# Kernel optimization log

Measured on AMD Instinct MI355X. Metric: run time of the kernel, lower is better.

The kernel has to match this reference:

```python
import jax, jax.numpy as jnp
import numpy as np

B, N, E = 2, 2048, 2048
HQ, HKV, D = 32, 8, 64
SCALE = 1.0 / np.sqrt(D)


def setup_inputs() -> dict:
    key = jax.random.key(0)
    ks = jax.random.split(key, 9)
    s = lambda k, shape, fan: jax.random.normal(k, shape, jnp.float32) / np.sqrt(fan)
    return {
        "x": jax.random.normal(ks[0], (B, N, E), jnp.float32),
        "Wq": s(ks[1], (HQ * D, E), E),
        "bq": jnp.zeros((HQ * D,), jnp.float32),
        "Wk": s(ks[2], (HKV * D, E), E),
        "bk": jnp.zeros((HKV * D,), jnp.float32),
        "Wv": s(ks[3], (HKV * D, E), E),
        "bv": jnp.zeros((HKV * D,), jnp.float32),
        "Wo": s(ks[4], (E, E), E),
        "bo": jnp.zeros((E,), jnp.float32),
    }


def _attention(x, Wq, bq, Wk, bk, Wv, bv, Wo, bo):
    G = HQ // HKV  # query heads per kv head
    # projections (torch Linear: y = x @ W.T + b)
    q = (jnp.einsum("bne,fe->bnf", x, Wq) + bq).reshape(B, N, HKV, G, D)
    k = (jnp.einsum("bne,fe->bnf", x, Wk) + bk).reshape(B, N, HKV, D)
    v = (jnp.einsum("bne,fe->bnf", x, Wv) + bv).reshape(B, N, HKV, D)
    # scores [B, HKV, G, N, N] -- GQA without materializing repeated K/V
    scores = jnp.einsum("bnhgd,bmhd->bhgnm", q, k) * SCALE
    causal = jnp.tril(jnp.ones((N, N), bool))
    scores = jnp.where(causal, scores, -jnp.inf)
    p = jax.nn.softmax(scores, axis=-1)
    o = jnp.einsum("bhgnm,bmhd->bnhgd", p, v).reshape(B, N, E)
    return jnp.einsum("bne,fe->bnf", o, Wo) + bo


def reference(x, Wq, bq, Wk, bk, Wv, bv, Wo, bo):
    return _attention(x, Wq, bq, Wk, bk, Wv, bv, Wo, bo)
```

## Files before the change

kernel.cpp:

```cpp
#include <hip/hip_runtime.h>
#include <hip/hip_bf16.h>


#define B_   2
#define N_   2048
#define E_   2048
#define HQ_  32
#define HKV_ 8
#define D_   64
#define BN_  (B_*N_)

typedef __attribute__((ext_vector_type(8))) short bf16x8;
typedef __attribute__((ext_vector_type(4))) float f32x4;

#define MFMA16(a,b,c) __builtin_amdgcn_mfma_f32_16x16x32_bf16(a,b,c,0,0,0)

__device__ inline unsigned short f2bf(float f) {
  unsigned u = __builtin_bit_cast(unsigned, f);
  u += 0x7FFFu + ((u >> 16) & 1u);
  return (unsigned short)(u >> 16);
}

__device__ inline unsigned pack_bf16_trunc(float lo, float hi) {
  return __builtin_amdgcn_perm(__builtin_bit_cast(unsigned, hi),
                               __builtin_bit_cast(unsigned, lo), 0x07060302u);
}

__device__ inline void gload_lds16(const void* g, void* l) {
  __builtin_amdgcn_global_load_lds(
      (const __attribute__((address_space(1))) void*)g,
      (__attribute__((address_space(3))) void*)l, 16, 0, 0);
}

__global__ void cast_all(const float* __restrict__ x,  const float* __restrict__ wq,
                         const float* __restrict__ wk, const float* __restrict__ wv,
                         const float* __restrict__ wo, unsigned short* __restrict__ dst) {
  const int c0 = 2097152;
  const int c1 = c0 + 1048576;
  const int c2 = c1 + 262144;
  const int c3 = c2 + 262144;
  const int c4 = c3 + 1048576;
  int i = blockIdx.x * blockDim.x + threadIdx.x;
  const int stride = gridDim.x * blockDim.x;
  for (; i < c4; i += stride) {
    const float* src; int off;
    if      (i < c0) { src = x;  off = i; }
    else if (i < c1) { src = wq; off = i - c0; }
    else if (i < c2) { src = wk; off = i - c1; }
    else if (i < c3) { src = wv; off = i - c2; }
    else             { src = wo; off = i - c3; }
    float4 f = reinterpret_cast<const float4*>(src)[off];
    ushort4 u;
    u.x = f2bf(f.x); u.y = f2bf(f.y); u.z = f2bf(f.z); u.w = f2bf(f.w);
    reinterpret_cast<ushort4*>(dst)[i] = u;
  }
}

__global__ __launch_bounds__(512, 4) void gemm_qkv(
    const unsigned short* __restrict__ A,
    const unsigned short* __restrict__ Wq, const unsigned short* __restrict__ Wk,
    const unsigned short* __restrict__ Wv,
    const float* __restrict__ bq, const float* __restrict__ bk, const float* __restrict__ bv,
    unsigned short* __restrict__ Qo, unsigned short* __restrict__ Ko,
    unsigned short* __restrict__ Vto)
{
  __shared__ __align__(16) unsigned short As[2][8192];
  __shared__ __align__(16) unsigned short Bs[2][12288];
  const int tid  = threadIdx.x;
  const int w    = tid >> 6;
  const int lane = tid & 63;
  const int g    = blockIdx.x & 7;
  const int s    = blockIdx.x >> 3;
  const int bm   = g*4 + (s >> 4);
  const int bn   = s & 15;
  const int m0   = bm << 7;
  const int n0v  = bn * 192;
  const int K    = E_;
  const float K2S = 0.125f * 1.44269504088896340736f;

  const int mgrp = w >> 2;
  const int ngrp = w & 3;
  const int cl   = lane & 15;
  const int kgrp = lane >> 4;
  const int rl   = kgrp << 2;
  const int li   = lane >> 3;
  const int lx   = lane & 7;

  const unsigned gsw = ((unsigned)(lx ^ li)) << 3;
  const unsigned short* gA = A + (size_t)(m0 + w*16 + li) * K + gsw;
  const unsigned short* gBq[3];
  #pragma unroll
  for (int q = 0; q < 3; ++q) {
    const int vr = n0v + w*24 + q*8;
    const unsigned short* base;
    if (vr < 2048)      base = Wq + (size_t)vr * K;
    else if (vr < 2560) base = Wk + (size_t)(vr - 2048) * K;
    else                base = Wv + (size_t)(vr - 2560) * K;
    gBq[q] = base + (size_t)li * K + gsw;
  }
  const unsigned aDst = (unsigned)(w*16)*64u + (unsigned)lane*8u;
  const unsigned bDst = (unsigned)(w*24)*64u + (unsigned)lane*8u;

  unsigned rAo[4][2], rBo[3][2];
  #pragma unroll
  for (int ks = 0; ks < 2; ++ks) {
    const unsigned c8 = (((unsigned)(ks*4 + kgrp)) ^ (unsigned)(cl & 7)) << 3;
    #pragma unroll
    for (int z = 0; z < 4; ++z)
      rAo[z][ks] = (unsigned)(mgrp*64 + z*16 + cl) * 64u + c8;
    #pragma unroll
    for (int jj = 0; jj < 3; ++jj)
      rBo[jj][ks] = (unsigned)(ngrp*48 + jj*16 + cl) * 64u + c8;
  }

  f32x4 acc[4][3] = {};
  const int nt = K >> 6;

  auto STAGE = [&](int kt, int buf) {
    const int ko = kt << 6;
    #pragma unroll
    for (int q = 0; q < 2; ++q)
      gload_lds16(gA + (size_t)(q*8)*K + ko, &As[buf][aDst + q*512u]);
    #pragma unroll
    for (int q = 0; q < 3; ++q)
      gload_lds16(gBq[q] + ko, &Bs[buf][bDst + q*512u]);
  };

  STAGE(0, 0);
  int p = 0;

  for (int t = 0; t < nt; ++t) {
    if (t + 1 < nt) {
      STAGE(t + 1, p ^ 1);
      asm volatile("s_waitcnt vmcnt(5)" ::: "memory");
    } else {
      asm volatile("s_waitcnt vmcnt(0)" ::: "memory");
    }
    __builtin_amdgcn_s_barrier();
    #pragma unroll
    for (int ks = 0; ks < 2; ++ks) {
      bf16x8 af[4], bfr[3];
      #pragma unroll
      for (int z = 0; z < 4; ++z)
        af[z] = *reinterpret_cast<const bf16x8*>(&As[p][rAo[z][ks]]);
      #pragma unroll
      for (int jj = 0; jj < 3; ++jj)
        bfr[jj] = *reinterpret_cast<const bf16x8*>(&Bs[p][rBo[jj][ks]]);
      __builtin_amdgcn_s_setprio(1);
      #pragma unroll
      for (int z = 0; z < 4; ++z)
        #pragma unroll
        for (int jj = 0; jj < 3; ++jj)
          acc[z][jj] = MFMA16(af[z], bfr[jj], acc[z][jj]);
      __builtin_amdgcn_s_setprio(0);
    }
    __builtin_amdgcn_s_barrier();
    p ^= 1;
  }

  #pragma unroll
  for (int z = 0; z < 4; ++z) {
    const int rowb = m0 + mgrp*64 + z*16 + rl;
    #pragma unroll
    for (int jj = 0; jj < 3; ++jj) {
      const int col16 = n0v + ngrp*48 + jj*16;
      if (col16 < 2048) {
        const int col = col16 + cl;
        const float bj = bq[col];
        #pragma unroll
        for (int r = 0; r < 4; ++r)
          Qo[(size_t)(rowb + r) * 2048 + col] = f2bf((acc[z][jj][r] + bj) * K2S);
      } else if (col16 < 2560) {
        const int col = col16 - 2048 + cl;
        const float bj = bk[col];
        #pragma unroll
        for (int r = 0; r < 4; ++r)
          Ko[(size_t)(rowb + r) * 512 + col] = f2bf(acc[z][jj][r] + bj);
      } else {
        const int col = col16 - 2560 + cl;
        const float bj = bv[col];
        ushort4 u;
        u.x = f2bf(acc[z][jj][0] + bj);
        u.y = f2bf(acc[z][jj][1] + bj);
        u.z = f2bf(acc[z][jj][2] + bj);
        u.w = f2bf(acc[z][jj][3] + bj);
        *reinterpret_cast<ushort4*>(&Vto[(size_t)col * 4096 + rowb]) = u;
      }
    }
  }
}

__global__ __launch_bounds__(256) void gemm_out(
    const unsigned short* __restrict__ A, const unsigned short* __restrict__ W,
    const float* __restrict__ bias, float* __restrict__ C)
{
  __shared__ __align__(16) unsigned short As[128*64];
  __shared__ __align__(16) unsigned short Bs[128*64];
  const int tid  = threadIdx.x;
  const int w    = tid >> 6;
  const int lane = tid & 63;
  const int bm   = blockIdx.x >> 4;
  const int bn   = blockIdx.x & 15;
  const int m0   = bm << 7, n0 = bn << 7;
  const int K    = E_;
  const int wr   = (w >> 1) << 6;
  const int wc   = (w & 1) << 6;
  const int cl   = lane & 15;
  const int kgrp = lane >> 4;
  const int rl   = kgrp << 2;
  const int li   = lane >> 3;
  const int lx   = lane & 7;

  const unsigned schunk = ((unsigned)(lx ^ li)) << 3;
  const unsigned short* gA = A + (size_t)(m0 + li) * K + schunk;
  const unsigned short* gB = W + (size_t)(n0 + li) * K + schunk;
  unsigned short* lA = As + lane*8;
  unsigned short* lB = Bs + lane*8;

  unsigned rA[4][2], rB[4][2];
  #pragma unroll
  for (int z = 0; z < 4; ++z)
    #pragma unroll
    for (int ks = 0; ks < 2; ++ks) {
      rA[z][ks] = (unsigned)(wr + z*16 + cl)*64u + ((((unsigned)ks*4u + (unsigned)kgrp) ^ (unsigned)(cl & 7)) << 3);
      rB[z][ks] = (unsigned)(wc + z*16 + cl)*64u + ((((unsigned)ks*4u + (unsigned)kgrp) ^ (unsigned)(cl & 7)) << 3);
    }

  f32x4 acc[4][4] = {};

  for (int kt = 0; kt < (K >> 6); ++kt) {
    const int ko = kt << 6;
    #pragma unroll
    for (int q = 0; q < 4; ++q) {
      const unsigned i = (unsigned)(w*4 + q);
      gload_lds16(gA + ((size_t)i*8*K + ko), lA + i*512);
      gload_lds16(gB + ((size_t)i*8*K + ko), lB + i*512);
    }
    __syncthreads();
    #pragma unroll
    for (int ks = 0; ks < 2; ++ks) {
      bf16x8 af[4], bfr[4];
      #pragma unroll
      for (int i = 0; i < 4; ++i)
        af[i] = *reinterpret_cast<const bf16x8*>(&As[rA[i][ks]]);
      #pragma unroll
      for (int j = 0; j < 4; ++j)
        bfr[j] = *reinterpret_cast<const bf16x8*>(&Bs[rB[j][ks]]);
      #pragma unroll
      for (int i = 0; i < 4; ++i)
        #pragma unroll
        for (int j = 0; j < 4; ++j)
          acc[i][j] = MFMA16(af[i], bfr[j], acc[i][j]);
    }
    __syncthreads();
  }

  #pragma unroll
  for (int j = 0; j < 4; ++j) {
    const int col = n0 + wc + j*16 + cl;
    const float bj = bias[col];
    #pragma unroll
    for (int i = 0; i < 4; ++i) {
      const int row = m0 + wr + i*16 + rl;
      #pragma unroll
      for (int r = 0; r < 4; ++r)
        C[(size_t)(row + r) * E_ + col] = acc[i][j][r] + bj;
    }
  }
}

__global__ __launch_bounds__(256, 3) void attn_kernel(
    const unsigned short* __restrict__ Q, const unsigned short* __restrict__ K,
    const unsigned short* __restrict__ Vt, unsigned short* __restrict__ O)
{
  __shared__ __align__(16) unsigned short Kbuf[2][4096];
  __shared__ __align__(16) unsigned short Vbuf[2][4096];
  __shared__ __align__(16) unsigned short Ps[4][2048];
  const int tid  = threadIdx.x;
  const int w    = tid >> 6;
  const int lane = tid & 63;
  const int bh   = blockIdx.x;
  const int b    = bh >> 3;
  const int h    = bh & 7;
  const int sidx = 63 - (int)blockIdx.y;
  const int hq   = h*4 + w;
  const int cl   = lane & 15;
  const int kgrp = lane >> 4;
  const int rl   = kgrp << 2;
  const int li   = lane >> 3;
  const int lx   = lane & 7;

  const float THR = 3.0f;

  char* pws = (char*)&Ps[w][0];
  const unsigned swz = ((unsigned)(cl & 7)) << 4;

  bf16x8 ones8;
  #pragma unroll
  for (int q = 0; q < 8; ++q) ones8[q] = (short)0x3F80;

  const char* Kp = (const char*)(K + (size_t)(b*N_)*512 + h*64);
  const char* Vp = (const char*)(Vt + (size_t)(h*64)*BN_ + b*N_);

  const unsigned schunk = ((unsigned)(lx ^ li)) << 4;
  const unsigned kso  = (unsigned)li*1024u + schunk;
  const unsigned vso  = (unsigned)li*8192u + schunk;
  const unsigned ldst = (unsigned)lane*16u;

  unsigned rdo[4][2];
  #pragma unroll
  for (int z = 0; z < 4; ++z)
    #pragma unroll
    for (int ks = 0; ks < 2; ++ks)
      rdo[z][ks] = (unsigned)z*2048u + (unsigned)cl*128u
                 + ((((unsigned)ks*4u + (unsigned)kgrp) ^ (unsigned)(cl & 7)) << 4);

  unsigned wb[2][4], rb[2][2];
  #pragma unroll
  for (int i = 0; i < 2; ++i) {
    #pragma unroll
    for (int c = 0; c < 4; ++c)
      wb[i][c] = (unsigned)i*2048u + (unsigned)cl*128u
               + (((unsigned)c*32u + (unsigned)kgrp*8u) ^ swz);
    #pragma unroll
    for (int ks = 0; ks < 2; ++ks)
      rb[i][ks] = (unsigned)i*2048u + (unsigned)cl*128u
                + (((unsigned)ks*64u + (unsigned)kgrp*16u) ^ swz);
  }

  const int q0 = sidx << 5;
  const int nt = (sidx >> 1) + 1;

  bf16x8 qf[2][2];
  #pragma unroll
  for (int i = 0; i < 2; ++i) {
    const size_t qoff = (size_t)(b*N_ + q0 + i*16 + cl) * E_ + hq*64 + (kgrp << 3);
    qf[i][0] = *reinterpret_cast<const bf16x8*>(Q + qoff);
    qf[i][1] = *reinterpret_cast<const bf16x8*>(Q + qoff + 32);
  }

  f32x4 o[2][4] = {};
  f32x4 l4[2] = {};
  float m[2] = {-1e30f, -1e30f};

  #pragma unroll
  for (int q = 0; q < 2; ++q) {
    const unsigned i = (unsigned)(w*2 + q);
    gload_lds16(Kp + (i*8192u + kso),  (char*)Kbuf[0] + (i*1024u + ldst));
    gload_lds16(Vp + (i*65536u + vso), (char*)Vbuf[0] + (i*1024u + ldst));
  }
  int cur = 0;
  __syncthreads();

  for (int t = 0; t < nt; ++t) {
    if (t + 1 < nt) {
      const unsigned kt = (unsigned)(t + 1) * 65536u;
      const unsigned vt = (unsigned)(t + 1) * 128u;
      #pragma unroll
      for (int q = 0; q < 2; ++q) {
        const unsigned i = (unsigned)(w*2 + q);
        gload_lds16(Kp + (kt + i*8192u + kso),  (char*)Kbuf[cur^1] + (i*1024u + ldst));
        gload_lds16(Vp + (vt + i*65536u + vso), (char*)Vbuf[cur^1] + (i*1024u + ldst));
      }
    }

    bf16x8 kf[4][2];
    #pragma unroll
    for (int c = 0; c < 4; ++c)
      #pragma unroll
      for (int ks = 0; ks < 2; ++ks)
        kf[c][ks] = *reinterpret_cast<const bf16x8*>((const char*)Kbuf[cur] + rdo[c][ks]);

    f32x4 s[2][4];
    #pragma unroll
    for (int i = 0; i < 2; ++i)
      #pragma unroll
      for (int c = 0; c < 4; ++c) {
        f32x4 z = {};
        z = MFMA16(kf[c][0], qf[i][0], z);
        z = MFMA16(kf[c][1], qf[i][1], z);
        s[i][c] = z;
      }

    if (t == nt - 1) {
      const int kvb = t << 6;
      #pragma unroll
      for (int i = 0; i < 2; ++i) {
        const int qq = q0 + i*16 + cl;
        #pragma unroll
        for (int c = 0; c < 4; ++c)
          #pragma unroll
          for (int r = 0; r < 4; ++r)
            if (kvb + c*16 + rl + r > qq) s[i][c][r] = -1e30f;
      }
    }

    #pragma unroll
    for (int i = 0; i < 2; ++i) {
      const float v0 = fmaxf(fmaxf(s[i][0][0], s[i][0][1]), s[i][0][2]);
      const float v1 = fmaxf(fmaxf(s[i][0][3], s[i][1][0]), s[i][1][1]);
      const float v2 = fmaxf(fmaxf(s[i][1][2], s[i][1][3]), s[i][2][0]);
      const float v3 = fmaxf(fmaxf(s[i][2][1], s[i][2][2]), s[i][2][3]);
      const float v4 = fmaxf(fmaxf(s[i][3][0], s[i][3][1]), s[i][3][2]);
      const float lm = fmaxf(fmaxf(fmaxf(v0, v1), v2),
                             fmaxf(fmaxf(v3, v4), s[i][3][3]));
      if (!__all(lm <= m[i] + THR)) {
        float tm = lm;
        tm = fmaxf(tm, __shfl_xor(tm, 16, 64));
        tm = fmaxf(tm, __shfl_xor(tm, 32, 64));
        const float mn = fmaxf(m[i], tm);
        const float al = __builtin_amdgcn_exp2f(m[i] - mn);
        m[i] = mn;
        l4[i] *= al;
        #pragma unroll
        for (int db = 0; db < 4; ++db) o[i][db] *= al;
      }
      const float mn = m[i];
      #pragma unroll
      for (int c = 0; c < 4; ++c) {
        const float e0 = __builtin_amdgcn_exp2f(s[i][c][0] - mn);
        const float e1 = __builtin_amdgcn_exp2f(s[i][c][1] - mn);
        const float e2 = __builtin_amdgcn_exp2f(s[i][c][2] - mn);
        const float e3 = __builtin_amdgcn_exp2f(s[i][c][3] - mn);
        uint2 u;
        u.x = pack_bf16_trunc(e0, e1);
        u.y = pack_bf16_trunc(e2, e3);
        *reinterpret_cast<uint2*>(pws + wb[i][c]) = u;
      }
    }

    bf16x8 vf[4][2];
    #pragma unroll
    for (int db = 0; db < 4; ++db)
      #pragma unroll
      for (int ks = 0; ks < 2; ++ks)
        vf[db][ks] = *reinterpret_cast<const bf16x8*>((const char*)Vbuf[cur] + rdo[db][ks]);

    #pragma unroll
    for (int i = 0; i < 2; ++i) {
      const bf16x8 pa0 = *reinterpret_cast<const bf16x8*>(pws + rb[i][0]);
      const bf16x8 pa1 = *reinterpret_cast<const bf16x8*>(pws + rb[i][1]);
      l4[i] = MFMA16(ones8, pa0, l4[i]);
      l4[i] = MFMA16(ones8, pa1, l4[i]);
      #pragma unroll
      for (int db = 0; db < 4; ++db) {
        o[i][db] = MFMA16(vf[db][0], pa0, o[i][db]);
        o[i][db] = MFMA16(vf[db][1], pa1, o[i][db]);
      }
    }

    __syncthreads();
    cur ^= 1;
  }

  #pragma unroll
  for (int i = 0; i < 2; ++i) {
    const float inv = 1.0f / l4[i][0];
    const size_t orow = (size_t)(b*N_ + q0 + i*16 + cl) * E_ + hq*64 + rl;
    #pragma unroll
    for (int db = 0; db < 4; ++db) {
      ushort4 u;
      u.x = f2bf(o[i][db][0] * inv);
      u.y = f2bf(o[i][db][1] * inv);
      u.z = f2bf(o[i][db][2] * inv);
      u.w = f2bf(o[i][db][3] * inv);
      *reinterpret_cast<ushort4*>(&O[orow + db*16]) = u;
    }
  }
}

extern "C" void kernel_launch(void* const* d_in, const int* in_sizes, int n_in,
                              void* d_out, int out_size, void* d_ws, size_t ws_size,
                              hipStream_t stream) {
  const float* x  = (const float*)d_in[0];
  const float* Wq = (const float*)d_in[1];
  const float* bq = (const float*)d_in[2];
  const float* Wk = (const float*)d_in[3];
  const float* bk = (const float*)d_in[4];
  const float* Wv = (const float*)d_in[5];
  const float* bv = (const float*)d_in[6];
  const float* Wo = (const float*)d_in[7];
  const float* bo = (const float*)d_in[8];
  float* out = (float*)d_out;

  unsigned short* ws  = (unsigned short*)d_ws;
  unsigned short* xb  = ws;
  unsigned short* Wqb = xb  + 8388608;
  unsigned short* Wkb = Wqb + 4194304;
  unsigned short* Wvb = Wkb + 1048576;
  unsigned short* Wob = Wvb + 1048576;
  unsigned short* Qb  = Wob + 4194304;
  unsigned short* Kb  = Qb  + 8388608;
  unsigned short* Vtb = Kb  + 2097152;
  unsigned short* Ob  = Vtb + 2097152;

  cast_all<<<dim3(2048), dim3(256), 0, stream>>>(x, Wq, Wk, Wv, Wo, xb);

  gemm_qkv<<<dim3(512), dim3(512), 0, stream>>>(xb, Wqb, Wkb, Wvb,
                                                bq, bk, bv, Qb, Kb, Vtb);

  attn_kernel<<<dim3(16, 64), dim3(256), 0, stream>>>(Qb, Kb, Vtb, Ob);

  gemm_out<<<dim3(32*16), dim3(256), 0, stream>>>(Ob, Wob, bo, out);
}
```

Before: 162.8 us.

## Double-buffer output GEMM with 512-thread blocks and grouped tile order

Rewrites the output projection GEMM to use 8 waves per 128x128 tile, each computing a 64x32 sub-tile. It double-buffers the LDS stages so the next K-slice loads overlap with the current MFMAs, and replaces the two __syncthreads per step with explicit vmcnt waits and barriers. Blocks are remapped into groups of 8 so neighbouring blocks share rows of A and get better L2 reuse, and setprio is raised around the MFMAs. LDS use doubles and the per-wave work halves, which trades fewer accumulator registers for more waves.

```diff
diff --git a/kernel.cpp b/kernel.cpp
--- a/kernel.cpp
+++ b/kernel.cpp
@@ -190,81 +190,103 @@
   }
 }
 
-__global__ __launch_bounds__(256) void gemm_out(
+__global__ __launch_bounds__(512, 4) void gemm_out(
     const unsigned short* __restrict__ A, const unsigned short* __restrict__ W,
     const float* __restrict__ bias, float* __restrict__ C)
 {
-  __shared__ __align__(16) unsigned short As[128*64];
-  __shared__ __align__(16) unsigned short Bs[128*64];
+  __shared__ __align__(16) unsigned short As[2][8192];
+  __shared__ __align__(16) unsigned short Bs[2][8192];
   const int tid  = threadIdx.x;
   const int w    = tid >> 6;
   const int lane = tid & 63;
-  const int bm   = blockIdx.x >> 4;
-  const int bn   = blockIdx.x & 15;
-  const int m0   = bm << 7, n0 = bn << 7;
+  const int g    = blockIdx.x & 7;
+  const int s    = blockIdx.x >> 3;
+  const int bm   = g*4 + (s >> 4);
+  const int bn   = s & 15;
+  const int m0   = bm << 7;
+  const int n0   = bn << 7;
   const int K    = E_;
-  const int wr   = (w >> 1) << 6;
-  const int wc   = (w & 1) << 6;
+
+  const int mgrp = w >> 2;
+  const int ngrp = w & 3;
   const int cl   = lane & 15;
   const int kgrp = lane >> 4;
   const int rl   = kgrp << 2;
   const int li   = lane >> 3;
   const int lx   = lane & 7;
 
-  const unsigned schunk = ((unsigned)(lx ^ li)) << 3;
-  const unsigned short* gA = A + (size_t)(m0 + li) * K + schunk;
-  const unsigned short* gB = W + (size_t)(n0 + li) * K + schunk;
-  unsigned short* lA = As + lane*8;
-  unsigned short* lB = Bs + lane*8;
-
-  unsigned rA[4][2], rB[4][2];
-  #pragma unroll
-  for (int z = 0; z < 4; ++z)
+  const unsigned gsw = ((unsigned)(lx ^ li)) << 3;
+  const unsigned short* gA = A + (size_t)(m0 + w*16 + li) * K + gsw;
+  const unsigned short* gB = W + (size_t)(n0 + w*16 + li) * K + gsw;
+  const unsigned dSt = (unsigned)(w*16)*64u + (unsigned)lane*8u;
+
+  unsigned rAo[4][2], rBo[2][2];
+  #pragma unroll
+  for (int ks = 0; ks < 2; ++ks) {
+    const unsigned c8 = (((unsigned)(ks*4 + kgrp)) ^ (unsigned)(cl & 7)) << 3;
+    #pragma unroll
+    for (int z = 0; z < 4; ++z)
+      rAo[z][ks] = (unsigned)(mgrp*64 + z*16 + cl) * 64u + c8;
+    #pragma unroll
+    for (int jj = 0; jj < 2; ++jj)
+      rBo[jj][ks] = (unsigned)(ngrp*32 + jj*16 + cl) * 64u + c8;
+  }
+
+  f32x4 acc[4][2] = {};
+  const int nt = K >> 6;
+
+  auto STAGE = [&](int kt, int buf) {
+    const int ko = kt << 6;
+    #pragma unroll
+    for (int q = 0; q < 2; ++q)
+      gload_lds16(gA + (size_t)(q*8)*K + ko, &As[buf][dSt + q*512u]);
+    #pragma unroll
+    for (int q = 0; q < 2; ++q)
+      gload_lds16(gB + (size_t)(q*8)*K + ko, &Bs[buf][dSt + q*512u]);
+  };
+
+  STAGE(0, 0);
+  int p = 0;
+
+  for (int t = 0; t < nt; ++t) {
+    if (t + 1 < nt) {
+      STAGE(t + 1, p ^ 1);
+      asm volatile("s_waitcnt vmcnt(4)" ::: "memory");
+    } else {
+      asm volatile("s_waitcnt vmcnt(0)" ::: "memory");
+    }
+    __builtin_amdgcn_s_barrier();
     #pragma unroll
     for (int ks = 0; ks < 2; ++ks) {
-      rA[z][ks] = (unsigned)(wr + z*16 + cl)*64u + ((((unsigned)ks*4u + (unsigned)kgrp) ^ (unsigned)(cl & 7)) << 3);
-      rB[z][ks] = (unsigned)(wc + z*16 + cl)*64u + ((((unsigned)ks*4u + (unsigned)kgrp) ^ (unsigned)(cl & 7)) << 3);
-    }
-
-  f32x4 acc[4][4] = {};
-
-  for (int kt = 0; kt < (K >> 6); ++kt) {
-    const int ko = kt << 6;
-    #pragma unroll
-    for (int q = 0; q < 4; ++q) {
-      const unsigned i = (unsigned)(w*4 + q);
-      gload_lds16(gA + ((size_t)i*8*K + ko), lA + i*512);
-      gload_lds16(gB + ((size_t)i*8*K + ko), lB + i*512);
-    }
-    __syncthreads();
-    #pragma unroll
-    for (int ks = 0; ks < 2; ++ks) {
-      bf16x8 af[4], bfr[4];
-      #pragma unroll
-      for (int i = 0; i < 4; ++i)
-        af[i] = *reinterpret_cast<const bf16x8*>(&As[rA[i][ks]]);
-      #pragma unroll
-      for (int j = 0; j < 4; ++j)
-        bfr[j] = *reinterpret_cast<const bf16x8*>(&Bs[rB[j][ks]]);
-      #pragma unroll
-      for (int i = 0; i < 4; ++i)
+      bf16x8 af[4], bfr[2];
+      #pragma unroll
+      for (int z = 0; z < 4; ++z)
+        af[z] = *reinterpret_cast<const bf16x8*>(&As[p][rAo[z][ks]]);
+      #pragma unroll
+      for (int jj = 0; jj < 2; ++jj)
+        bfr[jj] = *reinterpret_cast<const bf16x8*>(&Bs[p][rBo[jj][ks]]);
+      __builtin_amdgcn_s_setprio(1);
+      #pragma unroll
+      for (int z = 0; z < 4; ++z)
         #pragma unroll
-        for (int j = 0; j < 4; ++j)
-          acc[i][j] = MFMA16(af[i], bfr[j], acc[i][j]);
-    }
-    __syncthreads();
-  }
-
-  #pragma unroll
-  for (int j = 0; j < 4; ++j) {
-    const int col = n0 + wc + j*16 + cl;
-    const float bj = bias[col];
-    #pragma unroll
-    for (int i = 0; i < 4; ++i) {
-      const int row = m0 + wr + i*16 + rl;
+        for (int jj = 0; jj < 2; ++jj)
+          acc[z][jj] = MFMA16(af[z], bfr[jj], acc[z][jj]);
+      __builtin_amdgcn_s_setprio(0);
+    }
+    __builtin_amdgcn_s_barrier();
+    p ^= 1;
+  }
+
+  #pragma unroll
+  for (int z = 0; z < 4; ++z) {
+    const int rowb = m0 + mgrp*64 + z*16 + rl;
+    #pragma unroll
+    for (int jj = 0; jj < 2; ++jj) {
+      const int col = n0 + ngrp*32 + jj*16 + cl;
+      const float bj = bias[col];
       #pragma unroll
       for (int r = 0; r < 4; ++r)
-        C[(size_t)(row + r) * E_ + col] = acc[i][j][r] + bj;
+        C[(size_t)(rowb + r) * E_ + col] = acc[z][jj][r] + bj;
     }
   }
 }
@@ -501,5 +523,5 @@
 
   attn_kernel<<<dim3(16, 64), dim3(256), 0, stream>>>(Qb, Kb, Vtb, Ob);
 
-  gemm_out<<<dim3(32*16), dim3(256), 0, stream>>>(Ob, Wob, bo, out);
-}
+  gemm_out<<<dim3(512), dim3(512), 0, stream>>>(Ob, Wob, bo, out);
+}
```

Measured after the change: 158.0 us, median of 2. 3.0% less time.
